# Performance work log

Measured on AMD Instinct MI355X. Metric: run time of the kernel, lower is better.

The kernel has to match this reference:

```python
import jax, jax.numpy as jnp
import numpy as np

IN_DIM = 1024
INNER_DIM = 4096
HEADS = 16
HEAD_DIM = 64
EPS = 1e-5


def layer_norm(x, gamma, beta):
    mu = jnp.mean(x, axis=-1, keepdims=True)
    var = jnp.mean(jnp.square(x - mu), axis=-1, keepdims=True)
    return (x - mu) * jax.lax.rsqrt(var + EPS) * gamma + beta


def setup_inputs() -> dict:
    key = jax.random.key(0)
    ks = jax.random.split(key, 12)
    B, N = 2, 2048
    s_in = 1.0 / np.sqrt(IN_DIM)
    s_inner = 1.0 / np.sqrt(INNER_DIM)
    return {
        "x": jax.random.normal(ks[0], (B, N, IN_DIM), jnp.float32),
        "w_qkv": jax.random.normal(ks[1], (IN_DIM, HEADS * HEAD_DIM * 3), jnp.float32) * s_in,
        "b_qkv": jnp.zeros((HEADS * HEAD_DIM * 3,), jnp.float32),
        "w_proj": jax.random.normal(ks[2], (HEADS * HEAD_DIM, IN_DIM), jnp.float32) * s_in,
        "b_proj": jnp.zeros((IN_DIM,), jnp.float32),
        "g1": jnp.ones((IN_DIM,), jnp.float32),
        "beta1": jnp.zeros((IN_DIM,), jnp.float32),
        "w_ff1": jax.random.normal(ks[3], (IN_DIM, INNER_DIM), jnp.float32) * s_in,
        "b_ff1": jnp.zeros((INNER_DIM,), jnp.float32),
        "w_ff2": jax.random.normal(ks[4], (INNER_DIM, IN_DIM), jnp.float32) * s_inner,
        "b_ff2": jnp.zeros((IN_DIM,), jnp.float32),
        "g2": jnp.ones((IN_DIM,), jnp.float32),
        "beta2": jnp.zeros((IN_DIM,), jnp.float32),
    }


def reference(x, w_qkv, b_qkv, w_proj, b_proj, g1, beta1, w_ff1, b_ff1, w_ff2, b_ff2, g2, beta2):
    B, N, _ = x.shape
    scale = HEAD_DIM ** -0.5
    # QKV projection: (B,N,H,3D) -> (B,H,N,3D), then split as in torch chunk
    qkv = (x @ w_qkv + b_qkv).reshape(B, N, HEADS, 3 * HEAD_DIM).transpose(0, 2, 1, 3)
    q, k, v = jnp.split(qkv, 3, axis=-1)  # each (B,H,N,D)
    attn = jax.nn.softmax(jnp.einsum("bhnd,bhmd->bhnm", q, k) * scale, axis=-1)
    out = jnp.einsum("bhnm,bhmd->bhnd", attn, v).transpose(0, 2, 1, 3).reshape(B, N, HEADS * HEAD_DIM)
    out = out @ w_proj + b_proj
    # residual + LN1
    h = layer_norm(out + x, g1, beta1)
    # FFN + residual + LN2
    ff = jax.nn.relu(h @ w_ff1 + b_ff1) @ w_ff2 + b_ff2
    return layer_norm(ff + h, g2, beta2)
```

## Files before the change

kernel.cpp:

```cpp
#include <hip/hip_runtime.h>

typedef unsigned short u16;
typedef unsigned int u32;
typedef __attribute__((ext_vector_type(8))) short short8;
typedef __attribute__((ext_vector_type(4))) float float4v;

#define MB (1024 * 1024)

__device__ inline float b2f(u16 u) {
    union { u32 i; float f; } v; v.i = ((u32)u) << 16; return v.f;
}
__device__ inline u16 f2b(float f) {
    union { float f; u32 i; } v; v.f = f;
    u32 r = (v.i + 0x7FFF + ((v.i >> 16) & 1)) >> 16;
    return (u16)r;
}
__device__ inline u32 pk2(float a, float b) { return (u32)f2b(a) | ((u32)f2b(b) << 16); }

__global__ __launch_bounds__(256) void detect_dtype(const u16* __restrict__ x, u32* __restrict__ flag) {
    __shared__ int cnt;
    if (threadIdx.x == 0) cnt = 0;
    __syncthreads();
    int hits = 0;
    for (int i = threadIdx.x; i < 512; i += 256) {
        u16 w = x[2 * i];
        int e = (w >> 7) & 0xFF;
        if (e >= 116 && e <= 134) hits++;
    }
    atomicAdd(&cnt, hits);
    __syncthreads();
    if (threadIdx.x == 0) *flag = (cnt < 256) ? 1u : 0u;
}

__global__ __launch_bounds__(256) void convert_x(const void* __restrict__ src, u16* __restrict__ dst,
                                                 int n, const u32* __restrict__ flagp) {
    int i = (blockIdx.x * 256 + threadIdx.x) * 8;
    if (i >= n) return;
    if (*flagp) {
        const float* s = (const float*)src;
        float4 f0 = *(const float4*)(s + i);
        float4 f1 = *(const float4*)(s + i + 4);
        union { uint4 v; u16 u[8]; } O;
        O.u[0] = f2b(f0.x); O.u[1] = f2b(f0.y); O.u[2] = f2b(f0.z); O.u[3] = f2b(f0.w);
        O.u[4] = f2b(f1.x); O.u[5] = f2b(f1.y); O.u[6] = f2b(f1.z); O.u[7] = f2b(f1.w);
        *(uint4*)(dst + i) = O.v;
    } else {
        *(uint4*)(dst + i) = *(const uint4*)((const u16*)src + i);
    }
}

__global__ __launch_bounds__(256) void transpose_any(const void* __restrict__ src, u16* __restrict__ dst,
                                                     int ldS, int ldD, const u32* __restrict__ flagp) {
    __shared__ alignas(16) u16 tile[64 * 78];
    int c0 = blockIdx.x * 64, r0 = blockIdx.y * 64;
    int tid = threadIdx.x;
    u32 flg = *flagp;
#pragma unroll
    for (int it = 0; it < 2; ++it) {
        int idx = tid + it * 256;
        int rr = idx >> 3, cc = idx & 7;
        union { uint4 v; u16 u[8]; } U;
        if (flg) {
            const float* s = (const float*)src + (size_t)(r0 + rr) * ldS + c0 + cc * 8;
            float4 f0 = *(const float4*)(s);
            float4 f1 = *(const float4*)(s + 4);
            U.u[0] = f2b(f0.x); U.u[1] = f2b(f0.y); U.u[2] = f2b(f0.z); U.u[3] = f2b(f0.w);
            U.u[4] = f2b(f1.x); U.u[5] = f2b(f1.y); U.u[6] = f2b(f1.z); U.u[7] = f2b(f1.w);
        } else {
            U.v = *(const uint4*)((const u16*)src + (size_t)(r0 + rr) * ldS + c0 + cc * 8);
        }
#pragma unroll
        for (int j = 0; j < 8; ++j) tile[(cc * 8 + j) * 78 + rr] = U.u[j];
    }
    __syncthreads();
#pragma unroll
    for (int it = 0; it < 2; ++it) {
        int idx = tid + it * 256;
        int rr = idx >> 3, cc = idx & 7;
        const u32* t32 = (const u32*)(tile + rr * 78);
        uint4 v;
        v.x = t32[cc * 4 + 0]; v.y = t32[cc * 4 + 1]; v.z = t32[cc * 4 + 2]; v.w = t32[cc * 4 + 3];
        *(uint4*)(dst + (size_t)(c0 + rr) * ldD + r0 + cc * 8) = v;
    }
}

__global__ __launch_bounds__(256) void v_transpose(const u16* __restrict__ qkv, u16* __restrict__ vt) {
    __shared__ alignas(16) u16 tile[64 * 78];
    int n0 = blockIdx.x * 64;
    int bh = blockIdx.y, b = bh >> 4, h = bh & 15;
    const u16* src = qkv + (size_t)b * 2048 * 3072 + h * 192 + 128;
    int tid = threadIdx.x;
#pragma unroll
    for (int it = 0; it < 2; ++it) {
        int idx = tid + it * 256;
        int rr = idx >> 3, cc = idx & 7;
        union { uint4 v; u16 u[8]; } U;
        U.v = *(const uint4*)(src + (size_t)(n0 + rr) * 3072 + cc * 8);
#pragma unroll
        for (int j = 0; j < 8; ++j) tile[(cc * 8 + j) * 78 + rr] = U.u[j];
    }
    __syncthreads();
#pragma unroll
    for (int it = 0; it < 2; ++it) {
        int idx = tid + it * 256;
        int rr = idx >> 3, cc = idx & 7;
        const u32* t32 = (const u32*)(tile + rr * 78);
        uint4 v;
        v.x = t32[cc * 4 + 0]; v.y = t32[cc * 4 + 1]; v.z = t32[cc * 4 + 2]; v.w = t32[cc * 4 + 3];
        *(uint4*)(vt + ((size_t)bh * 64 + rr) * 2048 + n0 + cc * 8) = v;
    }
}

template <int BN>
__global__ __launch_bounds__(256) void gemm_bt(const u16* __restrict__ A, const u16* __restrict__ Bt,
                                               const void* __restrict__ bias, u16* __restrict__ Cb,
                                               float* __restrict__ Cf,
                                               int M, int N, int K, int relu,
                                               const u32* __restrict__ flagp) {
    __shared__ alignas(16) u16 sA[128 * 32];
    __shared__ alignas(16) u16 sB[BN * 32];
    constexpr int WMT = (BN == 128) ? 4 : 2;
    int tid = threadIdx.x;
    int n0 = blockIdx.x * BN, m0 = blockIdx.y * 128;
    int wave = tid >> 6, lane = tid & 63, l15 = lane & 15, quad = lane >> 4;
    int wm = (BN == 128) ? (wave >> 1) * 64 : wave * 32;
    int wn = (BN == 128) ? (wave & 1) * 64 : 0;
    float4v acc[WMT][4] = {};

    for (int k0 = 0; k0 < K; k0 += 32) {
        __syncthreads();
#pragma unroll
        for (int it = 0; it < 2; ++it) {
            int idx = it * 256 + tid;
            int rr = idx >> 2, kc = idx & 3;
            __builtin_amdgcn_global_load_lds(
                (const __attribute__((address_space(1))) void*)(A + (size_t)(m0 + rr) * K + k0 + kc * 8),
                (__attribute__((address_space(3))) void*)&sA[(it * 256 + wave * 64) * 8], 16, 0, 0);
        }
#pragma unroll
        for (int it = 0; it < BN / 64; ++it) {
            int idx = it * 256 + tid;
            int rr = idx >> 2, kc = idx & 3;
            __builtin_amdgcn_global_load_lds(
                (const __attribute__((address_space(1))) void*)(Bt + (size_t)(n0 + rr) * K + k0 + kc * 8),
                (__attribute__((address_space(3))) void*)&sB[(it * 256 + wave * 64) * 8], 16, 0, 0);
        }
        __syncthreads();
        short8 a[WMT], b[4];
#pragma unroll
        for (int mi = 0; mi < WMT; ++mi) a[mi] = *(const short8*)&sA[(wm + mi * 16 + l15) * 32 + quad * 8];
#pragma unroll
        for (int ni = 0; ni < 4; ++ni) b[ni] = *(const short8*)&sB[(wn + ni * 16 + l15) * 32 + quad * 8];
#pragma unroll
        for (int mi = 0; mi < WMT; ++mi)
#pragma unroll
            for (int ni = 0; ni < 4; ++ni)
                acc[mi][ni] = __builtin_amdgcn_mfma_f32_16x16x32_bf16(a[mi], b[ni], acc[mi][ni], 0, 0, 0);
    }
    u32 flg = *flagp;
#pragma unroll
    for (int ni = 0; ni < 4; ++ni) {
        int col = n0 + wn + ni * 16 + l15;
        float bv = flg ? ((const float*)bias)[col] : b2f(((const u16*)bias)[col]);
#pragma unroll
        for (int mi = 0; mi < WMT; ++mi) {
#pragma unroll
            for (int r = 0; r < 4; ++r) {
                int row = m0 + wm + mi * 16 + quad * 4 + r;
                float v = acc[mi][ni][r] + bv;
                if (relu) v = fmaxf(v, 0.f);
                if (Cf) Cf[(size_t)row * N + col] = v;
                else    Cb[(size_t)row * N + col] = f2b(v);
            }
        }
    }
}

__global__ __launch_bounds__(256) void attn_kernel(const u16* __restrict__ qkv, const u16* __restrict__ vt,
                                                   u16* __restrict__ outp) {
    __shared__ alignas(16) u16 sP[4][32 * 40];
    const float C2 = 0.18033688011112042f;
    int tid = threadIdx.x;
    int wave = tid >> 6, lane = tid & 63, l15 = lane & 15, quad = lane >> 4;
    int bh = blockIdx.y, b = bh >> 4, h = bh & 15;
    int m0 = blockIdx.x * 128 + wave * 32;
    const size_t hq = (size_t)b * 2048 * 3072 + (size_t)h * 192;
    const size_t hk = hq + 64;
    const u16* vbase = vt + (size_t)bh * 64 * 2048;
    u16* sp = sP[wave];

    short8 qf[2][2];
#pragma unroll
    for (int mt = 0; mt < 2; ++mt)
#pragma unroll
        for (int dc = 0; dc < 2; ++dc)
            qf[mt][dc] = *(const short8*)(qkv + hq + (size_t)(m0 + mt * 16 + l15) * 3072 + dc * 32 + quad * 8);

    float4v ot[4][2] = {};
    float mrun[2] = {-3e38f, -3e38f}, lrun[2] = {0.f, 0.f};

    short8 kf[2][2], vf[4];
#pragma unroll
    for (int nt = 0; nt < 2; ++nt)
#pragma unroll
        for (int dc = 0; dc < 2; ++dc)
            kf[nt][dc] = *(const short8*)(qkv + hk + (size_t)(nt * 16 + l15) * 3072 + dc * 32 + quad * 8);
#pragma unroll
    for (int dt = 0; dt < 4; ++dt)
        vf[dt] = *(const short8*)(vbase + (size_t)(dt * 16 + l15) * 2048 + quad * 8);

    for (int n0 = 0; n0 < 2048; n0 += 32) {
        short8 kn[2][2], vn[4];
        if (n0 + 32 < 2048) {
#pragma unroll
            for (int nt = 0; nt < 2; ++nt)
#pragma unroll
                for (int dc = 0; dc < 2; ++dc)
                    kn[nt][dc] = *(const short8*)(qkv + hk + (size_t)(n0 + 32 + nt * 16 + l15) * 3072 + dc * 32 + quad * 8);
#pragma unroll
            for (int dt = 0; dt < 4; ++dt)
                vn[dt] = *(const short8*)(vbase + (size_t)(dt * 16 + l15) * 2048 + n0 + 32 + quad * 8);
        }
        float4v st[2][2] = {};
#pragma unroll
        for (int nt = 0; nt < 2; ++nt)
#pragma unroll
            for (int mt = 0; mt < 2; ++mt)
#pragma unroll
                for (int dc = 0; dc < 2; ++dc)
                    st[nt][mt] = __builtin_amdgcn_mfma_f32_16x16x32_bf16(kf[nt][dc], qf[mt][dc], st[nt][mt], 0, 0, 0);

        float al[2];
#pragma unroll
        for (int mt = 0; mt < 2; ++mt) {
            float mx = fmaxf(fmaxf(fmaxf(st[0][mt][0], st[0][mt][1]), fmaxf(st[0][mt][2], st[0][mt][3])),
                             fmaxf(fmaxf(st[1][mt][0], st[1][mt][1]), fmaxf(st[1][mt][2], st[1][mt][3])));
            mx = fmaxf(mx, __shfl_xor(mx, 16));
            mx = fmaxf(mx, __shfl_xor(mx, 32));
            float mn = fmaxf(mrun[mt], mx);
            float alv = exp2f((mrun[mt] - mn) * C2);
            mrun[mt] = mn;
            float mterm = -mn * C2;
            float sm = 0.f;
#pragma unroll
            for (int nt = 0; nt < 2; ++nt) {
                float e0 = exp2f(__builtin_fmaf(st[nt][mt][0], C2, mterm));
                float e1 = exp2f(__builtin_fmaf(st[nt][mt][1], C2, mterm));
                float e2 = exp2f(__builtin_fmaf(st[nt][mt][2], C2, mterm));
                float e3 = exp2f(__builtin_fmaf(st[nt][mt][3], C2, mterm));
                sm += (e0 + e1) + (e2 + e3);
                *(uint2*)&sp[(mt * 16 + l15) * 40 + nt * 16 + quad * 4] = make_uint2(pk2(e0, e1), pk2(e2, e3));
            }
            sm += __shfl_xor(sm, 16);
            sm += __shfl_xor(sm, 32);
            lrun[mt] = lrun[mt] * alv + sm;
            al[mt] = alv;
        }
#pragma unroll
        for (int dt = 0; dt < 4; ++dt)
#pragma unroll
            for (int mt = 0; mt < 2; ++mt)
#pragma unroll
                for (int r = 0; r < 4; ++r) ot[dt][mt][r] *= al[mt];
        asm volatile("s_waitcnt lgkmcnt(0)" ::: "memory");
        short8 pb[2];
#pragma unroll
        for (int mt = 0; mt < 2; ++mt) pb[mt] = *(const short8*)&sp[(mt * 16 + l15) * 40 + quad * 8];
#pragma unroll
        for (int dt = 0; dt < 4; ++dt)
#pragma unroll
            for (int mt = 0; mt < 2; ++mt)
                ot[dt][mt] = __builtin_amdgcn_mfma_f32_16x16x32_bf16(vf[dt], pb[mt], ot[dt][mt], 0, 0, 0);
#pragma unroll
        for (int nt = 0; nt < 2; ++nt)
#pragma unroll
            for (int dc = 0; dc < 2; ++dc) kf[nt][dc] = kn[nt][dc];
#pragma unroll
        for (int dt = 0; dt < 4; ++dt) vf[dt] = vn[dt];
    }
#pragma unroll
    for (int mt = 0; mt < 2; ++mt) {
        float inv = 1.f / lrun[mt];
        size_t row = (size_t)b * 2048 + m0 + mt * 16 + l15;
#pragma unroll
        for (int dt = 0; dt < 4; ++dt) {
            u32 lo = pk2(ot[dt][mt][0] * inv, ot[dt][mt][1] * inv);
            u32 hi = pk2(ot[dt][mt][2] * inv, ot[dt][mt][3] * inv);
            *(uint2*)(outp + row * 1024 + h * 64 + dt * 16 + quad * 4) = make_uint2(lo, hi);
        }
    }
}

__device__ inline void ld4(const void* p, int mode, u32 flg, size_t base, float* d) {
    bool isf = (mode == 2) || (mode == 1 && flg);
    if (isf) {
        float4 t = *(const float4*)((const float*)p + base);
        d[0] = t.x; d[1] = t.y; d[2] = t.z; d[3] = t.w;
    } else {
        ushort4 u = *(const ushort4*)((const u16*)p + base);
        d[0] = b2f(u.x); d[1] = b2f(u.y); d[2] = b2f(u.z); d[3] = b2f(u.w);
    }
}

__global__ __launch_bounds__(256) void ln_kernel(const void* __restrict__ in1p, int m1,
                                                 const void* __restrict__ in2p, int m2,
                                                 const void* __restrict__ g, const void* __restrict__ bt,
                                                 void* __restrict__ outp, int mout,
                                                 const u32* __restrict__ flagp) {
    __shared__ float red[8];
    u32 flg = *flagp;
    int row = blockIdx.x, tid = threadIdx.x;
    size_t base = (size_t)row * 1024 + tid * 4;
    float a[4], c[4], vv[4];
    ld4(in1p, m1, flg, base, a);
    ld4(in2p, m2, flg, base, c);
#pragma unroll
    for (int j = 0; j < 4; ++j) vv[j] = a[j] + c[j];
    float s1 = vv[0] + vv[1] + vv[2] + vv[3];
    float s2 = vv[0] * vv[0] + vv[1] * vv[1] + vv[2] * vv[2] + vv[3] * vv[3];
#pragma unroll
    for (int off = 32; off; off >>= 1) { s1 += __shfl_xor(s1, off); s2 += __shfl_xor(s2, off); }
    int wv = tid >> 6;
    if ((tid & 63) == 0) { red[wv] = s1; red[4 + wv] = s2; }
    __syncthreads();
    float S1 = red[0] + red[1] + red[2] + red[3];
    float S2 = red[4] + red[5] + red[6] + red[7];
    float mu = S1 * (1.f / 1024.f);
    float var = S2 * (1.f / 1024.f) - mu * mu;
    float rs = rsqrtf(var + 1e-5f);
    int col = tid * 4;
    float gv[4], bv[4];
    ld4(g, 1, flg, col, gv);
    ld4(bt, 1, flg, col, bv);
    bool outf = (mout == 2) || (mout == 1 && flg);
#pragma unroll
    for (int j = 0; j < 4; ++j) {
        float ov = (vv[j] - mu) * rs * gv[j] + bv[j];
        if (outf) ((float*)outp)[(size_t)row * 1024 + col + j] = ov;
        else      ((u16*)outp)[(size_t)row * 1024 + col + j] = f2b(ov);
    }
}

extern "C" void kernel_launch(void* const* d_in, const int* in_sizes, int n_in,
                              void* d_out, int out_size, void* d_ws, size_t ws_size,
                              hipStream_t stream) {
    (void)in_sizes; (void)n_in; (void)out_size; (void)ws_size;
    const void* x      = d_in[0];
    const void* w_qkv  = d_in[1];
    const void* b_qkv  = d_in[2];
    const void* w_proj = d_in[3];
    const void* b_proj = d_in[4];
    const void* g1     = d_in[5];
    const void* beta1  = d_in[6];
    const void* w_ff1  = d_in[7];
    const void* b_ff1  = d_in[8];
    const void* w_ff2  = d_in[9];
    const void* b_ff2  = d_in[10];
    const void* g2     = d_in[11];
    const void* beta2  = d_in[12];

    char* ws = (char*)d_ws;
    u16*  x_bf16 = (u16*)(ws + 0);
    u16*  wqkvT  = (u16*)(ws + 8 * MB);
    u16*  vt     = (u16*)(ws + 8 * MB);
    u16*  wprojT = (u16*)(ws + 8 * MB);
    u16*  qkv    = (u16*)(ws + 16 * MB);
    float* projo = (float*)(ws + 16 * MB);
    u16*  ff1o   = (u16*)(ws + 8 * MB);
    u16*  attno  = (u16*)(ws + 40 * MB);
    u16*  hbuf   = (u16*)(ws + 40 * MB);
    u16*  wff1T  = (u16*)(ws + 0);
    u16*  wff2T  = (u16*)(ws + 0);
    u16*  ff2o   = (u16*)(ws + 48 * MB);
    u32*  flag   = (u32*)(ws + 56 * MB);

    detect_dtype<<<1, 256, 0, stream>>>((const u16*)x, flag);
    convert_x<<<2048, 256, 0, stream>>>(x, x_bf16, 4194304, flag);
    transpose_any<<<dim3(48, 16), 256, 0, stream>>>(w_qkv, wqkvT, 3072, 1024, flag);
    gemm_bt<128><<<dim3(24, 32), 256, 0, stream>>>(x_bf16, wqkvT, b_qkv, qkv, nullptr, 4096, 3072, 1024, 0, flag);
    v_transpose<<<dim3(32, 32), 256, 0, stream>>>(qkv, vt);
    attn_kernel<<<dim3(16, 32), 256, 0, stream>>>(qkv, vt, attno);
    transpose_any<<<dim3(16, 16), 256, 0, stream>>>(w_proj, wprojT, 1024, 1024, flag);
    gemm_bt<64><<<dim3(16, 32), 256, 0, stream>>>(attno, wprojT, b_proj, nullptr, projo, 4096, 1024, 1024, 0, flag);
    ln_kernel<<<4096, 256, 0, stream>>>(projo, 2, x_bf16, 0, g1, beta1, hbuf, 0, flag);
    transpose_any<<<dim3(64, 16), 256, 0, stream>>>(w_ff1, wff1T, 4096, 1024, flag);
    gemm_bt<128><<<dim3(32, 32), 256, 0, stream>>>(hbuf, wff1T, b_ff1, ff1o, nullptr, 4096, 4096, 1024, 1, flag);
    transpose_any<<<dim3(16, 64), 256, 0, stream>>>(w_ff2, wff2T, 1024, 4096, flag);
    gemm_bt<64><<<dim3(16, 32), 256, 0, stream>>>(ff1o, wff2T, b_ff2, ff2o, nullptr, 4096, 1024, 4096, 0, flag);
    ln_kernel<<<4096, 256, 0, stream>>>(ff2o, 0, hbuf, 0, g2, beta2, d_out, 1, flag);
}
```

Baseline: 476.6 us.

## Halve attention rows per wave, double-buffer K/V loads, skip unneeded rescales

The attention kernel now gives each wave 16 query rows instead of 32, which doubles the grid to 1024 blocks, and adds a launch_bounds occupancy hint of 4. K/V fragments for the next tile are loaded ahead in an unrolled two-stage loop. Softmax now uses the raw exp2 builtin, packs P to bf16 by truncation instead of round-to-nearest, and skips rescaling the output accumulators when no row maximum changed. In exchange, each K/V element is loaded twice as often per query row, truncation adds a little rounding error, and the last prefetch reads past the end of the sequence (the values are never used).

```diff
diff --git a/kernel.cpp b/kernel.cpp
--- a/kernel.cpp
+++ b/kernel.cpp
@@ -16,6 +16,9 @@
     return (u16)r;
 }
 __device__ inline u32 pk2(float a, float b) { return (u32)f2b(a) | ((u32)f2b(b) << 16); }
+__device__ inline u32 pk2t(float a, float b) {
+    return __builtin_amdgcn_perm(__float_as_uint(b), __float_as_uint(a), 0x07060302u);
+}
 
 __global__ __launch_bounds__(256) void detect_dtype(const u16* __restrict__ x, u32* __restrict__ flag) {
     __shared__ int cnt;
@@ -176,118 +179,97 @@
     }
 }
 
-__global__ __launch_bounds__(256) void attn_kernel(const u16* __restrict__ qkv, const u16* __restrict__ vt,
-                                                   u16* __restrict__ outp) {
-    __shared__ alignas(16) u16 sP[4][32 * 40];
+__global__ __launch_bounds__(256, 4) void attn_kernel(const u16* __restrict__ qkv, const u16* __restrict__ vt,
+                                                      u16* __restrict__ outp) {
+    __shared__ alignas(16) u16 sP[4][16 * 40];
     const float C2 = 0.18033688011112042f;
     int tid = threadIdx.x;
     int wave = tid >> 6, lane = tid & 63, l15 = lane & 15, quad = lane >> 4;
     int bh = blockIdx.y, b = bh >> 4, h = bh & 15;
-    int m0 = blockIdx.x * 128 + wave * 32;
+    int m0 = blockIdx.x * 64 + wave * 16;
     const size_t hq = (size_t)b * 2048 * 3072 + (size_t)h * 192;
-    const size_t hk = hq + 64;
-    const u16* vbase = vt + (size_t)bh * 64 * 2048;
+    const u16* kp0 = qkv + hq + 64 + (size_t)l15 * 3072 + quad * 8;
+    const u16* vp  = vt + (size_t)bh * 64 * 2048 + (size_t)l15 * 2048 + quad * 8;
     u16* sp = sP[wave];
 
-    short8 qf[2][2];
-#pragma unroll
-    for (int mt = 0; mt < 2; ++mt)
-#pragma unroll
-        for (int dc = 0; dc < 2; ++dc)
-            qf[mt][dc] = *(const short8*)(qkv + hq + (size_t)(m0 + mt * 16 + l15) * 3072 + dc * 32 + quad * 8);
-
-    float4v ot[4][2] = {};
-    float mrun[2] = {-3e38f, -3e38f}, lrun[2] = {0.f, 0.f};
-
-    short8 kf[2][2], vf[4];
-#pragma unroll
-    for (int nt = 0; nt < 2; ++nt)
-#pragma unroll
-        for (int dc = 0; dc < 2; ++dc)
-            kf[nt][dc] = *(const short8*)(qkv + hk + (size_t)(nt * 16 + l15) * 3072 + dc * 32 + quad * 8);
-#pragma unroll
-    for (int dt = 0; dt < 4; ++dt)
-        vf[dt] = *(const short8*)(vbase + (size_t)(dt * 16 + l15) * 2048 + quad * 8);
-
-    for (int n0 = 0; n0 < 2048; n0 += 32) {
-        short8 kn[2][2], vn[4];
-        if (n0 + 32 < 2048) {
-#pragma unroll
-            for (int nt = 0; nt < 2; ++nt)
-#pragma unroll
-                for (int dc = 0; dc < 2; ++dc)
-                    kn[nt][dc] = *(const short8*)(qkv + hk + (size_t)(n0 + 32 + nt * 16 + l15) * 3072 + dc * 32 + quad * 8);
+    short8 qf[2];
+#pragma unroll
+    for (int dc = 0; dc < 2; ++dc)
+        qf[dc] = *(const short8*)(qkv + hq + (size_t)(m0 + l15) * 3072 + dc * 32 + quad * 8);
+
+    float4v ot[4] = {};
+    float mrun = -3e38f, lrun = 0.f;
+
+    struct Frags { short8 k[2][2]; short8 v[4]; };
+    auto loadf = [&](int n0) {
+        Frags f;
+#pragma unroll
+        for (int nt = 0; nt < 2; ++nt)
+#pragma unroll
+            for (int dc = 0; dc < 2; ++dc)
+                f.k[nt][dc] = *(const short8*)(kp0 + (size_t)(n0 + nt * 16) * 3072 + dc * 32);
+#pragma unroll
+        for (int dt = 0; dt < 4; ++dt)
+            f.v[dt] = *(const short8*)(vp + (size_t)dt * 16 * 2048 + n0);
+        return f;
+    };
+
+    auto proc = [&](const Frags& f) {
+        float4v st0 = {}, st1 = {};
+        st0 = __builtin_amdgcn_mfma_f32_16x16x32_bf16(f.k[0][0], qf[0], st0, 0, 0, 0);
+        st0 = __builtin_amdgcn_mfma_f32_16x16x32_bf16(f.k[0][1], qf[1], st0, 0, 0, 0);
+        st1 = __builtin_amdgcn_mfma_f32_16x16x32_bf16(f.k[1][0], qf[0], st1, 0, 0, 0);
+        st1 = __builtin_amdgcn_mfma_f32_16x16x32_bf16(f.k[1][1], qf[1], st1, 0, 0, 0);
+        float mx = fmaxf(fmaxf(fmaxf(st0[0], st0[1]), fmaxf(st0[2], st0[3])),
+                         fmaxf(fmaxf(st1[0], st1[1]), fmaxf(st1[2], st1[3])));
+        mx = fmaxf(mx, __shfl_xor(mx, 16));
+        mx = fmaxf(mx, __shfl_xor(mx, 32));
+        float mold = mrun;
+        float mn = fmaxf(mold, mx);
+        mrun = mn;
+        float mterm = -mn * C2;
+        float e0 = __builtin_amdgcn_exp2f(__builtin_fmaf(st0[0], C2, mterm));
+        float e1 = __builtin_amdgcn_exp2f(__builtin_fmaf(st0[1], C2, mterm));
+        float e2 = __builtin_amdgcn_exp2f(__builtin_fmaf(st0[2], C2, mterm));
+        float e3 = __builtin_amdgcn_exp2f(__builtin_fmaf(st0[3], C2, mterm));
+        float e4 = __builtin_amdgcn_exp2f(__builtin_fmaf(st1[0], C2, mterm));
+        float e5 = __builtin_amdgcn_exp2f(__builtin_fmaf(st1[1], C2, mterm));
+        float e6 = __builtin_amdgcn_exp2f(__builtin_fmaf(st1[2], C2, mterm));
+        float e7 = __builtin_amdgcn_exp2f(__builtin_fmaf(st1[3], C2, mterm));
+        *(uint2*)&sp[l15 * 40 + quad * 4]      = make_uint2(pk2t(e0, e1), pk2t(e2, e3));
+        *(uint2*)&sp[l15 * 40 + 16 + quad * 4] = make_uint2(pk2t(e4, e5), pk2t(e6, e7));
+        float sm = ((e0 + e1) + (e2 + e3)) + ((e4 + e5) + (e6 + e7));
+        sm += __shfl_xor(sm, 16);
+        sm += __shfl_xor(sm, 32);
+        float alv = __builtin_amdgcn_exp2f((mold - mn) * C2);
+        lrun = lrun * alv + sm;
+        if (__any(mn > mold)) {
 #pragma unroll
             for (int dt = 0; dt < 4; ++dt)
-                vn[dt] = *(const short8*)(vbase + (size_t)(dt * 16 + l15) * 2048 + n0 + 32 + quad * 8);
-        }
-        float4v st[2][2] = {};
-#pragma unroll
-        for (int nt = 0; nt < 2; ++nt)
-#pragma unroll
-            for (int mt = 0; mt < 2; ++mt)
-#pragma unroll
-                for (int dc = 0; dc < 2; ++dc)
-                    st[nt][mt] = __builtin_amdgcn_mfma_f32_16x16x32_bf16(kf[nt][dc], qf[mt][dc], st[nt][mt], 0, 0, 0);
-
-        float al[2];
-#pragma unroll
-        for (int mt = 0; mt < 2; ++mt) {
-            float mx = fmaxf(fmaxf(fmaxf(st[0][mt][0], st[0][mt][1]), fmaxf(st[0][mt][2], st[0][mt][3])),
-                             fmaxf(fmaxf(st[1][mt][0], st[1][mt][1]), fmaxf(st[1][mt][2], st[1][mt][3])));
-            mx = fmaxf(mx, __shfl_xor(mx, 16));
-            mx = fmaxf(mx, __shfl_xor(mx, 32));
-            float mn = fmaxf(mrun[mt], mx);
-            float alv = exp2f((mrun[mt] - mn) * C2);
-            mrun[mt] = mn;
-            float mterm = -mn * C2;
-            float sm = 0.f;
-#pragma unroll
-            for (int nt = 0; nt < 2; ++nt) {
-                float e0 = exp2f(__builtin_fmaf(st[nt][mt][0], C2, mterm));
-                float e1 = exp2f(__builtin_fmaf(st[nt][mt][1], C2, mterm));
-                float e2 = exp2f(__builtin_fmaf(st[nt][mt][2], C2, mterm));
-                float e3 = exp2f(__builtin_fmaf(st[nt][mt][3], C2, mterm));
-                sm += (e0 + e1) + (e2 + e3);
-                *(uint2*)&sp[(mt * 16 + l15) * 40 + nt * 16 + quad * 4] = make_uint2(pk2(e0, e1), pk2(e2, e3));
-            }
-            sm += __shfl_xor(sm, 16);
-            sm += __shfl_xor(sm, 32);
-            lrun[mt] = lrun[mt] * alv + sm;
-            al[mt] = alv;
-        }
+#pragma unroll
+                for (int r = 0; r < 4; ++r) ot[dt][r] *= alv;
+        }
+        asm volatile("s_waitcnt lgkmcnt(0)" ::: "memory");
+        short8 pb = *(const short8*)&sp[l15 * 40 + quad * 8];
 #pragma unroll
         for (int dt = 0; dt < 4; ++dt)
-#pragma unroll
-            for (int mt = 0; mt < 2; ++mt)
-#pragma unroll
-                for (int r = 0; r < 4; ++r) ot[dt][mt][r] *= al[mt];
-        asm volatile("s_waitcnt lgkmcnt(0)" ::: "memory");
-        short8 pb[2];
-#pragma unroll
-        for (int mt = 0; mt < 2; ++mt) pb[mt] = *(const short8*)&sp[(mt * 16 + l15) * 40 + quad * 8];
-#pragma unroll
-        for (int dt = 0; dt < 4; ++dt)
-#pragma unroll
-            for (int mt = 0; mt < 2; ++mt)
-                ot[dt][mt] = __builtin_amdgcn_mfma_f32_16x16x32_bf16(vf[dt], pb[mt], ot[dt][mt], 0, 0, 0);
-#pragma unroll
-        for (int nt = 0; nt < 2; ++nt)
-#pragma unroll
-            for (int dc = 0; dc < 2; ++dc) kf[nt][dc] = kn[nt][dc];
-#pragma unroll
-        for (int dt = 0; dt < 4; ++dt) vf[dt] = vn[dt];
-    }
-#pragma unroll
-    for (int mt = 0; mt < 2; ++mt) {
-        float inv = 1.f / lrun[mt];
-        size_t row = (size_t)b * 2048 + m0 + mt * 16 + l15;
-#pragma unroll
-        for (int dt = 0; dt < 4; ++dt) {
-            u32 lo = pk2(ot[dt][mt][0] * inv, ot[dt][mt][1] * inv);
-            u32 hi = pk2(ot[dt][mt][2] * inv, ot[dt][mt][3] * inv);
-            *(uint2*)(outp + row * 1024 + h * 64 + dt * 16 + quad * 4) = make_uint2(lo, hi);
-        }
+            ot[dt] = __builtin_amdgcn_mfma_f32_16x16x32_bf16(f.v[dt], pb, ot[dt], 0, 0, 0);
+    };
+
+    Frags fA = loadf(0);
+    for (int n0 = 0; n0 < 2048; n0 += 64) {
+        Frags fB = loadf(n0 + 32);
+        proc(fA);
+        fA = loadf(n0 + 64);
+        proc(fB);
+    }
+    float inv = 1.f / lrun;
+    size_t row = (size_t)b * 2048 + m0 + l15;
+#pragma unroll
+    for (int dt = 0; dt < 4; ++dt) {
+        u32 lo = pk2(ot[dt][0] * inv, ot[dt][1] * inv);
+        u32 hi = pk2(ot[dt][2] * inv, ot[dt][3] * inv);
+        *(uint2*)(outp + row * 1024 + h * 64 + dt * 16 + quad * 4) = make_uint2(lo, hi);
     }
 }
 
@@ -379,7 +361,7 @@
     transpose_any<<<dim3(48, 16), 256, 0, stream>>>(w_qkv, wqkvT, 3072, 1024, flag);
     gemm_bt<128><<<dim3(24, 32), 256, 0, stream>>>(x_bf16, wqkvT, b_qkv, qkv, nullptr, 4096, 3072, 1024, 0, flag);
     v_transpose<<<dim3(32, 32), 256, 0, stream>>>(qkv, vt);
-    attn_kernel<<<dim3(16, 32), 256, 0, stream>>>(qkv, vt, attno);
+    attn_kernel<<<dim3(32, 32), 256, 0, stream>>>(qkv, vt, attno);
     transpose_any<<<dim3(16, 16), 256, 0, stream>>>(w_proj, wprojT, 1024, 1024, flag);
     gemm_bt<64><<<dim3(16, 32), 256, 0, stream>>>(attno, wprojT, b_proj, nullptr, projo, 4096, 1024, 1024, 0, flag);
     ln_kernel<<<4096, 256, 0, stream>>>(projo, 2, x_bf16, 0, g1, beta1, hbuf, 0, flag);
```

Result: slower. 586.7 us (+23.1%).

## Stage K/V tiles in LDS via async global-to-LDS loads in attention

Applied to the files above, without the earlier changes.

The attention kernel stops having each wave load its own copy of the K and V tiles from global memory into registers. Instead the block cooperatively stages each 32-key K/V tile into double-buffered, XOR-swizzled shared memory using global_load_lds, so the four waves share one load. It also uses the raw exp2 intrinsic, packs bf16 by truncation with a byte permute instead of round-to-nearest, and skips rescaling the output accumulator when the running max does not change. Costs include a block-wide barrier every iteration and slightly different bf16 rounding of the probabilities.

```diff
diff --git a/kernel.cpp b/kernel.cpp
--- a/kernel.cpp
+++ b/kernel.cpp
@@ -16,6 +16,9 @@
     return (u16)r;
 }
 __device__ inline u32 pk2(float a, float b) { return (u32)f2b(a) | ((u32)f2b(b) << 16); }
+__device__ inline u32 pk2t(float a, float b) {
+    return __builtin_amdgcn_perm(__float_as_uint(b), __float_as_uint(a), 0x07060302u);
+}
 
 __global__ __launch_bounds__(256) void detect_dtype(const u16* __restrict__ x, u32* __restrict__ flag) {
     __shared__ int cnt;
@@ -178,6 +181,8 @@
 
 __global__ __launch_bounds__(256) void attn_kernel(const u16* __restrict__ qkv, const u16* __restrict__ vt,
                                                    u16* __restrict__ outp) {
+    __shared__ alignas(16) u16 sK[2][32 * 64];
+    __shared__ alignas(16) u16 sV[2][64 * 32];
     __shared__ alignas(16) u16 sP[4][32 * 40];
     const float C2 = 0.18033688011112042f;
     int tid = threadIdx.x;
@@ -185,10 +190,23 @@
     int bh = blockIdx.y, b = bh >> 4, h = bh & 15;
     int m0 = blockIdx.x * 128 + wave * 32;
     const size_t hq = (size_t)b * 2048 * 3072 + (size_t)h * 192;
-    const size_t hk = hq + 64;
+    const u16* kbase = qkv + hq + 64;
     const u16* vbase = vt + (size_t)bh * 64 * 2048;
     u16* sp = sP[wave];
 
+    int kr = tid >> 3, kc = tid & 7;
+    int ksw = (kc ^ (kr & 7)) * 8;
+    int vr = tid >> 2, vc = tid & 3;
+    int vsw = (vc ^ ((vr + (vr >> 2)) & 3)) * 8;
+    auto stage = [&](int buf, int n0) {
+        __builtin_amdgcn_global_load_lds(
+            (const __attribute__((address_space(1))) void*)(kbase + (size_t)(n0 + kr) * 3072 + ksw),
+            (__attribute__((address_space(3))) void*)&sK[buf][wave * 8 * 64], 16, 0, 0);
+        __builtin_amdgcn_global_load_lds(
+            (const __attribute__((address_space(1))) void*)(vbase + (size_t)vr * 2048 + n0 + vsw),
+            (__attribute__((address_space(3))) void*)&sV[buf][wave * 16 * 32], 16, 0, 0);
+    };
+
     short8 qf[2][2];
 #pragma unroll
     for (int mt = 0; mt < 2; ++mt)
@@ -199,28 +217,26 @@
     float4v ot[4][2] = {};
     float mrun[2] = {-3e38f, -3e38f}, lrun[2] = {0.f, 0.f};
 
-    short8 kf[2][2], vf[4];
-#pragma unroll
-    for (int nt = 0; nt < 2; ++nt)
-#pragma unroll
-        for (int dc = 0; dc < 2; ++dc)
-            kf[nt][dc] = *(const short8*)(qkv + hk + (size_t)(nt * 16 + l15) * 3072 + dc * 32 + quad * 8);
-#pragma unroll
-    for (int dt = 0; dt < 4; ++dt)
-        vf[dt] = *(const short8*)(vbase + (size_t)(dt * 16 + l15) * 2048 + quad * 8);
-
-    for (int n0 = 0; n0 < 2048; n0 += 32) {
-        short8 kn[2][2], vn[4];
-        if (n0 + 32 < 2048) {
-#pragma unroll
-            for (int nt = 0; nt < 2; ++nt)
-#pragma unroll
-                for (int dc = 0; dc < 2; ++dc)
-                    kn[nt][dc] = *(const short8*)(qkv + hk + (size_t)(n0 + 32 + nt * 16 + l15) * 3072 + dc * 32 + quad * 8);
-#pragma unroll
-            for (int dt = 0; dt < 4; ++dt)
-                vn[dt] = *(const short8*)(vbase + (size_t)(dt * 16 + l15) * 2048 + n0 + 32 + quad * 8);
-        }
+    stage(0, 0);
+    for (int it = 0; it < 64; ++it) {
+        int buf = it & 1;
+        __syncthreads();
+        if (it + 1 < 64) stage(buf ^ 1, (it + 1) * 32);
+
+        short8 kf[2][2], vf[4];
+#pragma unroll
+        for (int nt = 0; nt < 2; ++nt)
+#pragma unroll
+            for (int dc = 0; dc < 2; ++dc) {
+                int row = nt * 16 + l15;
+                kf[nt][dc] = *(const short8*)&sK[buf][row * 64 + (((dc * 4 + quad) ^ (row & 7)) * 8)];
+            }
+#pragma unroll
+        for (int dt = 0; dt < 4; ++dt) {
+            int row = dt * 16 + l15;
+            vf[dt] = *(const short8*)&sV[buf][row * 32 + ((quad ^ ((row + (row >> 2)) & 3)) * 8)];
+        }
+
         float4v st[2][2] = {};
 #pragma unroll
         for (int nt = 0; nt < 2; ++nt)
@@ -230,38 +246,42 @@
                 for (int dc = 0; dc < 2; ++dc)
                     st[nt][mt] = __builtin_amdgcn_mfma_f32_16x16x32_bf16(kf[nt][dc], qf[mt][dc], st[nt][mt], 0, 0, 0);
 
-        float al[2];
+        float al[2]; bool up[2];
 #pragma unroll
         for (int mt = 0; mt < 2; ++mt) {
             float mx = fmaxf(fmaxf(fmaxf(st[0][mt][0], st[0][mt][1]), fmaxf(st[0][mt][2], st[0][mt][3])),
                              fmaxf(fmaxf(st[1][mt][0], st[1][mt][1]), fmaxf(st[1][mt][2], st[1][mt][3])));
             mx = fmaxf(mx, __shfl_xor(mx, 16));
             mx = fmaxf(mx, __shfl_xor(mx, 32));
-            float mn = fmaxf(mrun[mt], mx);
-            float alv = exp2f((mrun[mt] - mn) * C2);
+            float mold = mrun[mt];
+            float mn = fmaxf(mold, mx);
             mrun[mt] = mn;
             float mterm = -mn * C2;
             float sm = 0.f;
 #pragma unroll
             for (int nt = 0; nt < 2; ++nt) {
-                float e0 = exp2f(__builtin_fmaf(st[nt][mt][0], C2, mterm));
-                float e1 = exp2f(__builtin_fmaf(st[nt][mt][1], C2, mterm));
-                float e2 = exp2f(__builtin_fmaf(st[nt][mt][2], C2, mterm));
-                float e3 = exp2f(__builtin_fmaf(st[nt][mt][3], C2, mterm));
+                float e0 = __builtin_amdgcn_exp2f(__builtin_fmaf(st[nt][mt][0], C2, mterm));
+                float e1 = __builtin_amdgcn_exp2f(__builtin_fmaf(st[nt][mt][1], C2, mterm));
+                float e2 = __builtin_amdgcn_exp2f(__builtin_fmaf(st[nt][mt][2], C2, mterm));
+                float e3 = __builtin_amdgcn_exp2f(__builtin_fmaf(st[nt][mt][3], C2, mterm));
                 sm += (e0 + e1) + (e2 + e3);
-                *(uint2*)&sp[(mt * 16 + l15) * 40 + nt * 16 + quad * 4] = make_uint2(pk2(e0, e1), pk2(e2, e3));
+                *(uint2*)&sp[(mt * 16 + l15) * 40 + nt * 16 + quad * 4] =
+                    make_uint2(pk2t(e0, e1), pk2t(e2, e3));
             }
             sm += __shfl_xor(sm, 16);
             sm += __shfl_xor(sm, 32);
+            float alv = __builtin_amdgcn_exp2f((mold - mn) * C2);
             lrun[mt] = lrun[mt] * alv + sm;
             al[mt] = alv;
-        }
-#pragma unroll
-        for (int dt = 0; dt < 4; ++dt)
-#pragma unroll
-            for (int mt = 0; mt < 2; ++mt)
-#pragma unroll
-                for (int r = 0; r < 4; ++r) ot[dt][mt][r] *= al[mt];
+            up[mt] = __any(mn > mold);
+        }
+#pragma unroll
+        for (int mt = 0; mt < 2; ++mt)
+            if (up[mt])
+#pragma unroll
+                for (int dt = 0; dt < 4; ++dt)
+#pragma unroll
+                    for (int r = 0; r < 4; ++r) ot[dt][mt][r] *= al[mt];
         asm volatile("s_waitcnt lgkmcnt(0)" ::: "memory");
         short8 pb[2];
 #pragma unroll
@@ -271,12 +291,6 @@
 #pragma unroll
             for (int mt = 0; mt < 2; ++mt)
                 ot[dt][mt] = __builtin_amdgcn_mfma_f32_16x16x32_bf16(vf[dt], pb[mt], ot[dt][mt], 0, 0, 0);
-#pragma unroll
-        for (int nt = 0; nt < 2; ++nt)
-#pragma unroll
-            for (int dc = 0; dc < 2; ++dc) kf[nt][dc] = kn[nt][dc];
-#pragma unroll
-        for (int dt = 0; dt < 4; ++dt) vf[dt] = vn[dt];
     }
 #pragma unroll
     for (int mt = 0; mt < 2; ++mt) {
```

Result: faster. 446.3 us (-6.4%).
